# Kernel tuning notes

Measured on AMD Instinct MI355X. Metric: run time of the kernel, lower is better.

Reference implementation:

```python
import jax, jax.numpy as jnp
import numpy as np

TOP_K = 2
EPS = 1e-9


def setup_inputs() -> dict:
    key = jax.random.key(0)
    ks = jax.random.split(key, 5)
    B, S, D, H, E, G = 4, 2048, 1024, 1024, 8, 256
    x = jax.random.normal(ks[0], (B, S, D), dtype=jnp.float32)
    # gate MLP (top_k_gating with hidden_size=gating_size)
    Wg1 = jax.random.normal(ks[1], (D, G), dtype=jnp.float32) * (1.0 / np.sqrt(D))
    Wg2 = jax.random.normal(ks[2], (G, E), dtype=jnp.float32) * (1.0 / np.sqrt(G))
    # experts: uniform(-1/D, 1/D) as in init_experts
    W_in = jax.random.uniform(ks[3], (E, D, H), dtype=jnp.float32, minval=-1.0 / D, maxval=1.0 / D)
    W_out = jax.random.uniform(ks[4], (E, H, D), dtype=jnp.float32, minval=-1.0 / D, maxval=1.0 / D)
    return {"x": x, "Wg1": Wg1, "Wg2": Wg2, "W_in": W_in, "W_out": W_out}


def _gate(xf, Wg1, Wg2):
    # gate MLP -> softmax probs over experts
    h = jnp.tanh(xf @ Wg1)                      # [N, G]
    probs = jax.nn.softmax(h @ Wg2, axis=-1)    # [N, E]
    top_v, top_i = jax.lax.top_k(probs, TOP_K)  # [N, k]
    N, E = probs.shape
    # dense gate matrix: zeros except top-k entries (== compute_gating combine weights)
    gates = jnp.zeros((N, E), probs.dtype).at[jnp.arange(N)[:, None], top_i].set(top_v)
    return gates, probs


def _mi_loss(probs):
    # mutual-information aux loss: minimize -(H(mean_p) - mean H(p))
    p_mean = probs.mean(axis=0)
    h_mean = -jnp.sum(p_mean * jnp.log(p_mean + EPS))
    mean_h = -jnp.mean(jnp.sum(probs * jnp.log(probs + EPS), axis=-1))
    return -h_mean + mean_h


def reference(x, Wg1, Wg2, W_in, W_out):
    B, S, D = x.shape
    xf = x.reshape(-1, D)                        # [N, D]
    gates, probs = _gate(xf, Wg1, Wg2)           # [N, E]
    # per-expert FFN: relu(x @ W_in[e]) @ W_out[e], combined with top-k gates.
    h = jnp.einsum('nd,edh->enh', xf, W_in)      # [E, N, H]
    h = jax.nn.relu(h)
    y = jnp.einsum('enh,ehd->end', h, W_out)     # [E, N, D]
    out = jnp.einsum('ne,end->nd', gates, y)     # gate-weighted combine
    loss = _mi_loss(probs)
    return out.reshape(B, S, D), loss
```

## Files before the change

### kernel.cpp

```cpp
#include <hip/hip_runtime.h>


#define N_TOK 8192
#define DIM   1024
#define HID   1024
#define NEXP  8
#define GDIM  256
#define NPAIR (N_TOK * 2)
#define HB_ROWS (NPAIR + 256)
#define MT2   72
#define GAP_P 5e-4f
#define SPLIT_SCALE 2048.0f

typedef __attribute__((ext_vector_type(4))) float    f32x4;
typedef __attribute__((ext_vector_type(8))) _Float16 f16x8;

static __device__ __forceinline__ void async_ld16(const void* g, void* l) {
  __builtin_amdgcn_global_load_lds(
      (const __attribute__((address_space(1))) unsigned int*)g,
      (__attribute__((address_space(3))) unsigned int*)l, 16, 0, 0);
}

__global__ __launch_bounds__(256) void prep_kernel(const float* __restrict__ x,
                                                   _Float16* __restrict__ xh,
                                                   _Float16* __restrict__ xl,
                                                   const float* __restrict__ Wg1,
                                                   _Float16* __restrict__ WhT,
                                                   _Float16* __restrict__ WlT,
                                                   const float* __restrict__ Win,
                                                   const float* __restrict__ Wout,
                                                   _Float16* __restrict__ WinT,
                                                   _Float16* __restrict__ WoutT) {
  __shared__ float t[64][65];
  int bx = blockIdx.x;
  int tid = threadIdx.x;
  if (bx < 4096) {
    size_t o = ((size_t)bx * 256 + tid) * 8;
    float4 v0 = *(const float4*)(x + o);
    float4 v1 = *(const float4*)(x + o + 4);
    float v[8] = {v0.x, v0.y, v0.z, v0.w, v1.x, v1.y, v1.z, v1.w};
    f16x8 h, l;
#pragma unroll
    for (int k = 0; k < 8; ++k) {
      _Float16 hi = (_Float16)v[k];
      h[k] = hi;
      l[k] = (_Float16)((v[k] - (float)hi) * SPLIT_SCALE);
    }
    *(f16x8*)(xh + o) = h;
    *(f16x8*)(xl + o) = l;
  } else if (bx < 4096 + 64) {
    int b = bx - 4096;
    int k0 = (b & 15) * 64, g0 = (b >> 4) * 64;
    int col4 = tid & 15, ib = tid >> 4;
#pragma unroll
    for (int q = 0; q < 4; ++q) {
      int i = ib * 4 + q;
      *(float4*)&t[i][col4 * 4] = *(const float4*)&Wg1[(size_t)(k0 + i) * GDIM + g0 + col4 * 4];
    }
    __syncthreads();
#pragma unroll
    for (int q = 0; q < 2; ++q) {
      int c = tid * 2 + q;
      int j = c >> 3, i8 = (c & 7) * 8;
      f16x8 h, l;
#pragma unroll
      for (int k = 0; k < 8; ++k) {
        float v = t[i8 + k][j];
        _Float16 hi = (_Float16)v;
        h[k] = hi;
        l[k] = (_Float16)((v - (float)hi) * SPLIT_SCALE);
      }
      *(f16x8*)&WhT[(size_t)(g0 + j) * DIM + k0 + i8] = h;
      *(f16x8*)&WlT[(size_t)(g0 + j) * DIM + k0 + i8] = l;
    }
  } else {
    int b = bx - 4160;
    int z = b >> 8, rem = b & 255;
    const float* src = (z < NEXP ? Win : Wout) + (size_t)(z & 7) * DIM * HID;
    _Float16*    dst = (z < NEXP ? WinT : WoutT) + (size_t)(z & 7) * DIM * HID;
    int i0 = (rem & 15) * 64, j0 = (rem >> 4) * 64;
    int col4 = tid & 15, ib = tid >> 4;
#pragma unroll
    for (int q = 0; q < 4; ++q) {
      int i = ib * 4 + q;
      *(float4*)&t[i][col4 * 4] = *(const float4*)&src[(size_t)(i0 + i) * 1024 + j0 + col4 * 4];
    }
    __syncthreads();
#pragma unroll
    for (int q = 0; q < 2; ++q) {
      int c = tid * 2 + q;
      int j = c >> 3, i8 = (c & 7) * 8;
      f16x8 h;
#pragma unroll
      for (int k = 0; k < 8; ++k) h[k] = (_Float16)t[i8 + k][j];
      *(f16x8*)&dst[(size_t)(j0 + j) * 1024 + i0 + i8] = h;
    }
  }
}

__global__ __launch_bounds__(256) void gemm_hm_kernel(const _Float16* __restrict__ xh,
                                                      const _Float16* __restrict__ xl,
                                                      const _Float16* __restrict__ WhT,
                                                      const _Float16* __restrict__ WlT,
                                                      float* __restrict__ hg) {
  __shared__ __align__(16) _Float16 Ah[32 * 32], Al[32 * 32];
  __shared__ __align__(16) _Float16 Bh[128 * 32], Bl[128 * 32];
  int m0 = blockIdx.x * 32, n0 = blockIdx.y * 128;
  int tid = threadIdx.x, lane = tid & 63, wave = tid >> 6;
  int wr = (wave >> 1) * 16, wc = (wave & 1) * 64;
  int sel = tid >> 7, tt = tid & 127;
  int arow = tt >> 2;
  int aslot = (tt & 3) ^ ((tt >> 4) & 3);
  const _Float16* asrcp = (sel ? xl : xh) + (size_t)(m0 + arow) * DIM + aslot * 8;
  _Float16* adst = (sel ? Al : Ah) + (size_t)tt * 8;
  int brow = tid >> 2;
  int bslot = (tid & 3) ^ ((tid >> 4) & 3);
  size_t boff = (size_t)(n0 + brow) * DIM + bslot * 8;
  const size_t bo2 = (size_t)64 * DIM;
  int rdoff = ((lane >> 4) ^ ((lane >> 2) & 3)) << 3;
  f32x4 acc[4] = {}, accl[4] = {};
  for (int k0 = 0; k0 < DIM; k0 += 32) {
    __syncthreads();
    async_ld16(asrcp + k0, adst);
    async_ld16(WhT + boff + k0, Bh + (size_t)tid * 8);
    async_ld16(WhT + boff + bo2 + k0, Bh + (size_t)(256 + tid) * 8);
    async_ld16(WlT + boff + k0, Bl + (size_t)tid * 8);
    async_ld16(WlT + boff + bo2 + k0, Bl + (size_t)(256 + tid) * 8);
    __syncthreads();
    f16x8 a  = *(const f16x8*)&Ah[(wr + (lane & 15)) * 32 + rdoff];
    f16x8 al = *(const f16x8*)&Al[(wr + (lane & 15)) * 32 + rdoff];
#pragma unroll
    for (int n = 0; n < 4; ++n) {
      f16x8 b  = *(const f16x8*)&Bh[(wc + n * 16 + (lane & 15)) * 32 + rdoff];
      f16x8 bl = *(const f16x8*)&Bl[(wc + n * 16 + (lane & 15)) * 32 + rdoff];
      acc[n]  = __builtin_amdgcn_mfma_f32_16x16x32_f16(a, b, acc[n], 0, 0, 0);
      accl[n] = __builtin_amdgcn_mfma_f32_16x16x32_f16(al, b, accl[n], 0, 0, 0);
      accl[n] = __builtin_amdgcn_mfma_f32_16x16x32_f16(a, bl, accl[n], 0, 0, 0);
    }
  }
#pragma unroll
  for (int n = 0; n < 4; ++n) {
#pragma unroll
    for (int i = 0; i < 4; ++i) {
      int row = wr + ((lane >> 4) << 2) + i;
      int col = wc + n * 16 + (lane & 15);
      float v = acc[n][i] + accl[n][i] * (1.0f / SPLIT_SCALE);
      hg[(size_t)(m0 + row) * GDIM + n0 + col] = tanhf(v);
    }
  }
}

__global__ void gate_kernel(const float* __restrict__ hg, const float* __restrict__ Wg2,
                            int* __restrict__ top_i, float* __restrict__ top_v,
                            float* __restrict__ lossacc, int* __restrict__ counts,
                            int* __restrict__ nflag, int* __restrict__ flaglist) {
  __shared__ float psum[8];
  __shared__ float entsum;
  __shared__ int cnts[8];
  int tid = threadIdx.x;
  if (tid < 8) { psum[tid] = 0.f; cnts[tid] = 0; }
  if (tid == 0) entsum = 0.f;
  __syncthreads();
  int token = blockIdx.x * 8 + (tid >> 5);
  int lane = tid & 31;
  const float* hrow = hg + (size_t)token * GDIM;
  float lg[8] = {0, 0, 0, 0, 0, 0, 0, 0};
#pragma unroll
  for (int j = 0; j < 8; ++j) {
    int g = lane + (j << 5);
    float hv = hrow[g];
#pragma unroll
    for (int e = 0; e < 8; ++e) lg[e] = fmaf(hv, Wg2[g * 8 + e], lg[e]);
  }
#pragma unroll
  for (int e = 0; e < 8; ++e) {
    lg[e] += __shfl_xor(lg[e], 16);
    lg[e] += __shfl_xor(lg[e], 8);
    lg[e] += __shfl_xor(lg[e], 4);
    lg[e] += __shfl_xor(lg[e], 2);
    lg[e] += __shfl_xor(lg[e], 1);
  }
  if (lane == 0) {
    float mx = lg[0];
#pragma unroll
    for (int e = 1; e < 8; ++e) mx = fmaxf(mx, lg[e]);
    float p[8], s = 0.f;
#pragma unroll
    for (int e = 0; e < 8; ++e) { p[e] = expf(lg[e] - mx); s += p[e]; }
    float inv = 1.f / s, ent = 0.f;
    int i0 = 0, i1 = 0;
    float v0 = -1.f, v1 = -1.f, v2 = -1.f;
#pragma unroll
    for (int e = 0; e < 8; ++e) {
      p[e] *= inv;
      ent += p[e] * logf(p[e] + 1e-9f);
      if (p[e] > v0)      { v2 = v1; v1 = v0; i1 = i0; v0 = p[e]; i0 = e; }
      else if (p[e] > v1) { v2 = v1; v1 = p[e]; i1 = e; }
      else if (p[e] > v2) { v2 = p[e]; }
    }
    top_i[token * 2 + 0] = i0; top_i[token * 2 + 1] = i1;
    top_v[token * 2 + 0] = v0; top_v[token * 2 + 1] = v1;
    if (v1 - v2 < GAP_P) {
      int ix = atomicAdd(nflag, 1);
      if (ix < 8192) flaglist[ix] = token;
    }
#pragma unroll
    for (int e = 0; e < 8; ++e) atomicAdd(&psum[e], p[e]);
    atomicAdd(&entsum, ent);
    atomicAdd(&cnts[i0], 1);
    atomicAdd(&cnts[i1], 1);
  }
  __syncthreads();
  if (tid < 8) { atomicAdd(&lossacc[tid], psum[tid]); atomicAdd(&counts[tid], cnts[tid]); }
  if (tid == 8) atomicAdd(&lossacc[8], entsum);
}

__global__ __launch_bounds__(256) void regate_kernel(const float* __restrict__ x,
                                                     const float* __restrict__ Wg1,
                                                     const float* __restrict__ Wg2,
                                                     const int* __restrict__ nflag,
                                                     const int* __restrict__ flaglist,
                                                     int* __restrict__ top_i,
                                                     float* __restrict__ top_v,
                                                     int* __restrict__ counts) {
  __shared__ float xs[DIM];
  __shared__ float wsum[4][8];
  int tid = threadIdx.x;
  int nf = *nflag; if (nf > 8192) nf = 8192;
  for (int it = blockIdx.x; it < nf; it += gridDim.x) {
    int token = flaglist[it];
    const float* xr = x + (size_t)token * DIM;
    *(float4*)&xs[tid * 4] = *(const float4*)&xr[tid * 4];
    __syncthreads();
    float s0 = 0.f, s1 = 0.f, s2 = 0.f, s3 = 0.f;
    float s4 = 0.f, s5 = 0.f, s6 = 0.f, s7 = 0.f;
    for (int k = 0; k < DIM; k += 8) {
      s0 = fmaf(xs[k + 0], Wg1[(size_t)(k + 0) * GDIM + tid], s0);
      s1 = fmaf(xs[k + 1], Wg1[(size_t)(k + 1) * GDIM + tid], s1);
      s2 = fmaf(xs[k + 2], Wg1[(size_t)(k + 2) * GDIM + tid], s2);
      s3 = fmaf(xs[k + 3], Wg1[(size_t)(k + 3) * GDIM + tid], s3);
      s4 = fmaf(xs[k + 4], Wg1[(size_t)(k + 4) * GDIM + tid], s4);
      s5 = fmaf(xs[k + 5], Wg1[(size_t)(k + 5) * GDIM + tid], s5);
      s6 = fmaf(xs[k + 6], Wg1[(size_t)(k + 6) * GDIM + tid], s6);
      s7 = fmaf(xs[k + 7], Wg1[(size_t)(k + 7) * GDIM + tid], s7);
    }
    float hgv = tanhf(((s0 + s1) + (s2 + s3)) + ((s4 + s5) + (s6 + s7)));
    float lg[8];
#pragma unroll
    for (int e = 0; e < 8; ++e) lg[e] = hgv * Wg2[tid * 8 + e];
#pragma unroll
    for (int e = 0; e < 8; ++e) {
      lg[e] += __shfl_xor(lg[e], 32);
      lg[e] += __shfl_xor(lg[e], 16);
      lg[e] += __shfl_xor(lg[e], 8);
      lg[e] += __shfl_xor(lg[e], 4);
      lg[e] += __shfl_xor(lg[e], 2);
      lg[e] += __shfl_xor(lg[e], 1);
    }
    int wv = tid >> 6;
    if ((tid & 63) == 0) {
#pragma unroll
      for (int e = 0; e < 8; ++e) wsum[wv][e] = lg[e];
    }
    __syncthreads();
    if (tid == 0) {
      float l[8];
#pragma unroll
      for (int e = 0; e < 8; ++e)
        l[e] = (wsum[0][e] + wsum[1][e]) + (wsum[2][e] + wsum[3][e]);
      float mx = l[0];
#pragma unroll
      for (int e = 1; e < 8; ++e) mx = fmaxf(mx, l[e]);
      float p[8], s = 0.f;
#pragma unroll
      for (int e = 0; e < 8; ++e) { p[e] = expf(l[e] - mx); s += p[e]; }
      float inv = 1.f / s;
      int i0 = 0, i1 = 0;
      float v0 = -1.f, v1 = -1.f;
#pragma unroll
      for (int e = 0; e < 8; ++e) {
        p[e] *= inv;
        if (p[e] > v0)      { v1 = v0; i1 = i0; v0 = p[e]; i0 = e; }
        else if (p[e] > v1) { v1 = p[e]; i1 = e; }
      }
      int oi0 = top_i[token * 2 + 0], oi1 = top_i[token * 2 + 1];
      if (oi0 != i0 || oi1 != i1) {
        atomicSub(&counts[oi0], 1); atomicSub(&counts[oi1], 1);
        atomicAdd(&counts[i0], 1);  atomicAdd(&counts[i1], 1);
      }
      top_i[token * 2 + 0] = i0; top_i[token * 2 + 1] = i1;
      top_v[token * 2 + 0] = v0; top_v[token * 2 + 1] = v1;
    }
    __syncthreads();
  }
}

__global__ __launch_bounds__(256) void fill_kernel(const int* __restrict__ top_i,
                                                   const float* __restrict__ top_v,
                                                   const int* __restrict__ counts,
                                                   int* __restrict__ cursors,
                                                   int* __restrict__ ptok,
                                                   float* __restrict__ pgate,
                                                   int* __restrict__ rowof) {
  __shared__ int lcnt[8];
  __shared__ int lbase[8];
  __shared__ int soff[8];
  int tid = threadIdx.x;
  int n = blockIdx.x * 256 + tid;
  if (tid == 0) {
    int a = 0;
#pragma unroll
    for (int e = 0; e < 8; ++e) { soff[e] = a; a += counts[e]; }
  }
  if (tid < 8) lcnt[tid] = 0;
  __syncthreads();
  int e0 = top_i[n * 2 + 0], e1 = top_i[n * 2 + 1];
  int p0 = atomicAdd(&lcnt[e0], 1);
  int p1 = atomicAdd(&lcnt[e1], 1);
  __syncthreads();
  if (tid < 8) lbase[tid] = atomicAdd(&cursors[tid], lcnt[tid]);
  __syncthreads();
  int r0 = soff[e0] + lbase[e0] + p0;
  int r1 = soff[e1] + lbase[e1] + p1;
  ptok[r0] = n;  pgate[r0] = top_v[n * 2 + 0];  rowof[n * 2 + 0] = r0;
  ptok[r1] = n;  pgate[r1] = top_v[n * 2 + 1];  rowof[n * 2 + 1] = r1;
}


#define GEMM_PIPE(STAGE_EXPR)                                                        \
  STAGE_EXPR(0, 0);                                                                  \
  STAGE_EXPR(32, 1);                                                                 \
  asm volatile("s_waitcnt vmcnt(3)" ::: "memory");                                   \
  __builtin_amdgcn_s_barrier();                                                      \
  int cbuf = 0;                                                                      \
  for (int t = 0; t < 32; ++t) {                                                     \
    f16x8 a[4], b[4];                                                                \
    _Pragma("unroll")                                                                \
    for (int m = 0; m < 4; ++m)                                                      \
      a[m] = *(const f16x8*)&Als[cbuf][(wr + m * 16 + (lane & 15)) * 32 + rdoff];    \
    _Pragma("unroll")                                                                \
    for (int n = 0; n < 4; ++n)                                                      \
      b[n] = *(const f16x8*)&Bls[cbuf][(wc + n * 16 + (lane & 15)) * 32 + rdoff];    \
    asm volatile("s_waitcnt lgkmcnt(0)" ::: "memory");                               \
    __builtin_amdgcn_sched_barrier(0);                                               \
    __builtin_amdgcn_s_barrier();                                                    \
    bool st = (t + 2 < 32);                                                          \
    if (st) { STAGE_EXPR((t + 2) * 32, cbuf); }                                      \
    __builtin_amdgcn_s_setprio(1);                                                   \
    _Pragma("unroll")                                                                \
    for (int m = 0; m < 4; ++m)                                                      \
      _Pragma("unroll")                                                              \
      for (int n = 0; n < 4; ++n)                                                    \
        acc[m][n] = __builtin_amdgcn_mfma_f32_16x16x32_f16(a[m], b[n], acc[m][n], 0, 0, 0); \
    __builtin_amdgcn_s_setprio(0);                                                   \
    if (st) asm volatile("s_waitcnt vmcnt(3)" ::: "memory");                         \
    else    asm volatile("s_waitcnt vmcnt(0)" ::: "memory");                         \
    __builtin_amdgcn_sched_barrier(0);                                               \
    __builtin_amdgcn_s_barrier();                                                    \
    cbuf ^= 1;                                                                       \
  }

__global__ __launch_bounds__(512) void gemm1_kernel(const _Float16* __restrict__ xh,
                                                    const _Float16* __restrict__ WinT,
                                                    _Float16* __restrict__ hb,
                                                    const int* __restrict__ counts,
                                                    const int* __restrict__ ptok) {
  __shared__ __align__(16) _Float16 Als[2][256 * 32];
  __shared__ __align__(16) _Float16 Bls[2][128 * 32];
  int bx = blockIdx.x;
  int loc = (bx & 7) * 9 + (bx >> 3);
  int base = 0, cnt = 0, e;
  for (e = 0; e < NEXP; ++e) {
    cnt = counts[e];
    int mts = (cnt + 255) >> 8;
    if (loc < mts) break;
    loc -= mts; base += cnt;
  }
  if (e == NEXP) return;
  int row0 = base + (loc << 8);
  int rmax = cnt - (loc << 8);
  int n0 = blockIdx.y << 7;
  int tid = threadIdx.x, wave = tid >> 6, lane = tid & 63;
  int wr = (wave >> 1) << 6, wc = (wave & 1) << 6;

  const _Float16* WB = WinT + (size_t)e * DIM * HID;
  int scol = (((lane & 3) ^ (lane >> 4)) << 3);
  size_t asrc[2];
#pragma unroll
  for (int j = 0; j < 2; ++j) {
    int r = wave * 32 + j * 16 + (lane >> 2);
    int tok = ptok[(r < rmax) ? (row0 + r) : base];
    asrc[j] = (size_t)tok * DIM + scol;
  }
  int brow = tid >> 2;
  size_t bsrc = (size_t)(n0 + brow) * DIM + (((tid & 3) ^ ((tid >> 4) & 3)) << 3);
  int aldst = wave * 1024;
  int bldst = wave * 512;
  int rdoff = ((lane >> 4) ^ ((lane >> 2) & 3)) << 3;
  f32x4 acc[4][4] = {};

#define STAGE1(K0, CB)                                          \
  do {                                                          \
    async_ld16(xh + asrc[0] + (K0), &Als[(CB)][aldst]);         \
    async_ld16(xh + asrc[1] + (K0), &Als[(CB)][aldst + 512]);   \
    async_ld16(WB + bsrc + (K0), &Bls[(CB)][bldst]);            \
  } while (0)

  GEMM_PIPE(STAGE1)
#undef STAGE1

#pragma unroll
  for (int m = 0; m < 4; ++m) {
#pragma unroll
    for (int i = 0; i < 4; ++i) {
      int r = wr + m * 16 + ((lane >> 4) << 2) + i;
      if (r < rmax) {
        _Float16* hrow = hb + (size_t)(row0 + r) * HID;
#pragma unroll
        for (int n = 0; n < 4; ++n)
          hrow[n0 + wc + n * 16 + (lane & 15)] = (_Float16)fmaxf(acc[m][n][i], 0.f);
      }
    }
  }
}

__global__ __launch_bounds__(512) void gemm2_kernel(const _Float16* __restrict__ hb,
                                                    const _Float16* __restrict__ WoutT,
                                                    _Float16* __restrict__ yb,
                                                    const int* __restrict__ counts,
                                                    const float* __restrict__ pgate) {
  __shared__ __align__(16) _Float16 Als[2][256 * 32];
  __shared__ __align__(16) _Float16 Bls[2][128 * 32];
  int bx = blockIdx.x;
  int loc = (bx & 7) * 9 + (bx >> 3);
  int base = 0, cnt = 0, e;
  for (e = 0; e < NEXP; ++e) {
    cnt = counts[e];
    int mts = (cnt + 255) >> 8;
    if (loc < mts) break;
    loc -= mts; base += cnt;
  }
  if (e == NEXP) return;
  int row0 = base + (loc << 8);
  int rmax = cnt - (loc << 8);
  int n0 = blockIdx.y << 7;
  int tid = threadIdx.x, wave = tid >> 6, lane = tid & 63;
  int wr = (wave >> 1) << 6, wc = (wave & 1) << 6;

  const _Float16* WB = WoutT + (size_t)e * DIM * HID;
  int scol = (((lane & 3) ^ (lane >> 4)) << 3);
  size_t asrc[2];
#pragma unroll
  for (int j = 0; j < 2; ++j) {
    int r = wave * 32 + j * 16 + (lane >> 2);
    asrc[j] = (size_t)(row0 + r) * HID + scol;
  }
  int brow = tid >> 2;
  size_t bsrc = (size_t)(n0 + brow) * DIM + (((tid & 3) ^ ((tid >> 4) & 3)) << 3);
  int aldst = wave * 1024;
  int bldst = wave * 512;
  int rdoff = ((lane >> 4) ^ ((lane >> 2) & 3)) << 3;
  f32x4 acc[4][4] = {};

#define STAGE2(K0, CB)                                          \
  do {                                                          \
    async_ld16(hb + asrc[0] + (K0), &Als[(CB)][aldst]);         \
    async_ld16(hb + asrc[1] + (K0), &Als[(CB)][aldst + 512]);   \
    async_ld16(WB + bsrc + (K0), &Bls[(CB)][bldst]);            \
  } while (0)

  GEMM_PIPE(STAGE2)
#undef STAGE2

#pragma unroll
  for (int m = 0; m < 4; ++m) {
#pragma unroll
    for (int i = 0; i < 4; ++i) {
      int r = wr + m * 16 + ((lane >> 4) << 2) + i;
      if (r < rmax) {
        int gr = row0 + r;
        float gv = pgate[gr];
        _Float16* yrow = yb + (size_t)gr * DIM;
#pragma unroll
        for (int n = 0; n < 4; ++n)
          yrow[n0 + wc + n * 16 + (lane & 15)] = (_Float16)(gv * acc[m][n][i]);
      }
    }
  }
}

__global__ __launch_bounds__(256) void combine_kernel(const _Float16* __restrict__ yb,
                                                      const int* __restrict__ rowof,
                                                      float* __restrict__ out,
                                                      const float* __restrict__ lossacc,
                                                      float* __restrict__ lossdst) {
  int tid = threadIdx.x;
  int token = blockIdx.x * 2 + (tid >> 7);
  int d0 = (tid & 127) * 8;
  int r0 = rowof[token * 2 + 0];
  int r1 = rowof[token * 2 + 1];
  f16x8 a = *(const f16x8*)&yb[(size_t)r0 * DIM + d0];
  f16x8 b = *(const f16x8*)&yb[(size_t)r1 * DIM + d0];
  float* orow = out + (size_t)token * DIM + d0;
  float4 o0, o1;
  o0.x = (float)a[0] + (float)b[0]; o0.y = (float)a[1] + (float)b[1];
  o0.z = (float)a[2] + (float)b[2]; o0.w = (float)a[3] + (float)b[3];
  o1.x = (float)a[4] + (float)b[4]; o1.y = (float)a[5] + (float)b[5];
  o1.z = (float)a[6] + (float)b[6]; o1.w = (float)a[7] + (float)b[7];
  *(float4*)orow = o0;
  *(float4*)(orow + 4) = o1;
  if (blockIdx.x == 0 && tid == 0) {
    float t1 = 0.f;
#pragma unroll
    for (int e = 0; e < 8; ++e) {
      float pm = lossacc[e] * (1.f / (float)N_TOK);
      t1 += pm * logf(pm + 1e-9f);
    }
    lossdst[0] = t1 - lossacc[8] * (1.f / (float)N_TOK);
  }
}

extern "C" void kernel_launch(void* const* d_in, const int* in_sizes, int n_in,
                              void* d_out, int out_size, void* d_ws, size_t ws_size,
                              hipStream_t stream) {
  const float* x    = (const float*)d_in[0];
  const float* Wg1  = (const float*)d_in[1];
  const float* Wg2  = (const float*)d_in[2];
  const float* Win  = (const float*)d_in[3];
  const float* Wout = (const float*)d_in[4];
  float* out = (float*)d_out;

  char* ws = (char*)d_ws;
  size_t off = 0;
  auto alloc = [&](size_t bytes) -> void* {
    void* p = ws + off;
    off = (off + bytes + 255) & ~(size_t)255;
    return p;
  };
  int*   counts  = (int*)alloc(32);
  int*   cursors = (int*)alloc(32);
  float* lossacc = (float*)alloc(64);
  int*   nflag   = (int*)alloc(32);
  int*   flaglist= (int*)alloc(8192 * 4);
  int*   top_i   = (int*)alloc((size_t)NPAIR * 4);
  float* top_v   = (float*)alloc((size_t)NPAIR * 4);
  int*   ptok    = (int*)alloc((size_t)NPAIR * 4);
  float* pgate   = (float*)alloc((size_t)NPAIR * 4);
  int*   rowof   = (int*)alloc((size_t)NPAIR * 4);
  float* hg      = (float*)alloc((size_t)N_TOK * GDIM * 4);
  char*  scratch1 = (char*)alloc((size_t)HB_ROWS * HID * 2);
  _Float16* xl     = (_Float16*)scratch1;
  _Float16* Wg1hT  = (_Float16*)(scratch1 + (size_t)N_TOK * DIM * 2);
  _Float16* Wg1lsT = Wg1hT + (size_t)GDIM * DIM;
  _Float16* hb     = (_Float16*)scratch1;
  _Float16* xh    = (_Float16*)alloc((size_t)N_TOK * DIM * 2);
  _Float16* WinT  = (_Float16*)alloc((size_t)NEXP * DIM * HID * 2);
  _Float16* WoutT = (_Float16*)alloc((size_t)NEXP * DIM * HID * 2);
  _Float16* yb = xh;
  (void)ws_size; (void)in_sizes; (void)n_in;

  hipMemsetAsync(d_ws, 0, 2048, stream);

  prep_kernel<<<4096 + 64 + 4096, 256, 0, stream>>>(x, xh, xl, Wg1, Wg1hT, Wg1lsT,
                                                    Win, Wout, WinT, WoutT);
  gemm_hm_kernel<<<dim3(N_TOK / 32, GDIM / 128), 256, 0, stream>>>(xh, xl, Wg1hT, Wg1lsT, hg);
  gate_kernel<<<N_TOK / 8, 256, 0, stream>>>(hg, Wg2, top_i, top_v, lossacc, counts,
                                             nflag, flaglist);
  regate_kernel<<<256, 256, 0, stream>>>(x, Wg1, Wg2, nflag, flaglist, top_i, top_v, counts);
  fill_kernel<<<N_TOK / 256, 256, 0, stream>>>(top_i, top_v, counts, cursors,
                                               ptok, pgate, rowof);
  gemm1_kernel<<<dim3(MT2, HID / 128), 512, 0, stream>>>(xh, WinT, hb, counts, ptok);
  gemm2_kernel<<<dim3(MT2, DIM / 128), 512, 0, stream>>>(hb, WoutT, yb, counts, pgate);
  combine_kernel<<<N_TOK / 2, 256, 0, stream>>>(yb, rowof, out, lossacc,
                                                out + (size_t)N_TOK * DIM);
}
```

Before: 261.5 us.

## Halve GEMM workgroup to 4 waves with 128x64 per-wave tiles

Both expert GEMM kernels now use 256 threads (4 waves) instead of 512 for the same 256x128 block tile. Each wave computes a 128x64 sub-tile with 8x4 MFMA accumulators and issues six async loads per stage, and the vmcnt waits are updated to match. The aim is more register-level reuse of A/B fragments per LDS read and fewer waves synchronising at barriers. The cost is doubled accumulator register pressure, which with launch_bounds(256,2) may limit occupancy or cause spills.

```diff
diff --git a/kernel.cpp b/kernel.cpp
--- a/kernel.cpp
+++ b/kernel.cpp
@@ -330,13 +330,13 @@
 #define GEMM_PIPE(STAGE_EXPR)                                                        \
   STAGE_EXPR(0, 0);                                                                  \
   STAGE_EXPR(32, 1);                                                                 \
-  asm volatile("s_waitcnt vmcnt(3)" ::: "memory");                                   \
+  asm volatile("s_waitcnt vmcnt(6)" ::: "memory");                                   \
   __builtin_amdgcn_s_barrier();                                                      \
   int cbuf = 0;                                                                      \
   for (int t = 0; t < 32; ++t) {                                                     \
-    f16x8 a[4], b[4];                                                                \
+    f16x8 a[8], b[4];                                                                \
     _Pragma("unroll")                                                                \
-    for (int m = 0; m < 4; ++m)                                                      \
+    for (int m = 0; m < 8; ++m)                                                      \
       a[m] = *(const f16x8*)&Als[cbuf][(wr + m * 16 + (lane & 15)) * 32 + rdoff];    \
     _Pragma("unroll")                                                                \
     for (int n = 0; n < 4; ++n)                                                      \
@@ -348,23 +348,23 @@
     if (st) { STAGE_EXPR((t + 2) * 32, cbuf); }                                      \
     __builtin_amdgcn_s_setprio(1);                                                   \
     _Pragma("unroll")                                                                \
-    for (int m = 0; m < 4; ++m)                                                      \
+    for (int m = 0; m < 8; ++m)                                                      \
       _Pragma("unroll")                                                              \
       for (int n = 0; n < 4; ++n)                                                    \
         acc[m][n] = __builtin_amdgcn_mfma_f32_16x16x32_f16(a[m], b[n], acc[m][n], 0, 0, 0); \
     __builtin_amdgcn_s_setprio(0);                                                   \
-    if (st) asm volatile("s_waitcnt vmcnt(3)" ::: "memory");                         \
+    if (st) asm volatile("s_waitcnt vmcnt(6)" ::: "memory");                         \
     else    asm volatile("s_waitcnt vmcnt(0)" ::: "memory");                         \
     __builtin_amdgcn_sched_barrier(0);                                               \
     __builtin_amdgcn_s_barrier();                                                    \
     cbuf ^= 1;                                                                       \
   }
 
-__global__ __launch_bounds__(512) void gemm1_kernel(const _Float16* __restrict__ xh,
-                                                    const _Float16* __restrict__ WinT,
-                                                    _Float16* __restrict__ hb,
-                                                    const int* __restrict__ counts,
-                                                    const int* __restrict__ ptok) {
+__global__ __launch_bounds__(256, 2) void gemm1_kernel(const _Float16* __restrict__ xh,
+                                                       const _Float16* __restrict__ WinT,
+                                                       _Float16* __restrict__ hb,
+                                                       const int* __restrict__ counts,
+                                                       const int* __restrict__ ptok) {
   __shared__ __align__(16) _Float16 Als[2][256 * 32];
   __shared__ __align__(16) _Float16 Bls[2][128 * 32];
   int bx = blockIdx.x;
@@ -381,36 +381,42 @@
   int rmax = cnt - (loc << 8);
   int n0 = blockIdx.y << 7;
   int tid = threadIdx.x, wave = tid >> 6, lane = tid & 63;
-  int wr = (wave >> 1) << 6, wc = (wave & 1) << 6;
+  int wr = (wave >> 1) << 7;
+  int wc = (wave & 1) << 6;
 
   const _Float16* WB = WinT + (size_t)e * DIM * HID;
   int scol = (((lane & 3) ^ (lane >> 4)) << 3);
-  size_t asrc[2];
-#pragma unroll
-  for (int j = 0; j < 2; ++j) {
-    int r = wave * 32 + j * 16 + (lane >> 2);
+  size_t asrc[4];
+#pragma unroll
+  for (int j = 0; j < 4; ++j) {
+    int r = wave * 64 + j * 16 + (lane >> 2);
     int tok = ptok[(r < rmax) ? (row0 + r) : base];
     asrc[j] = (size_t)tok * DIM + scol;
   }
-  int brow = tid >> 2;
-  size_t bsrc = (size_t)(n0 + brow) * DIM + (((tid & 3) ^ ((tid >> 4) & 3)) << 3);
-  int aldst = wave * 1024;
-  int bldst = wave * 512;
+  size_t bsrc[2];
+#pragma unroll
+  for (int j = 0; j < 2; ++j) {
+    int r = j * 64 + (tid >> 2);
+    bsrc[j] = (size_t)(n0 + r) * DIM + (((tid & 3) ^ ((tid >> 4) & 3)) << 3);
+  }
   int rdoff = ((lane >> 4) ^ ((lane >> 2) & 3)) << 3;
-  f32x4 acc[4][4] = {};
-
-#define STAGE1(K0, CB)                                          \
-  do {                                                          \
-    async_ld16(xh + asrc[0] + (K0), &Als[(CB)][aldst]);         \
-    async_ld16(xh + asrc[1] + (K0), &Als[(CB)][aldst + 512]);   \
-    async_ld16(WB + bsrc + (K0), &Bls[(CB)][bldst]);            \
+  f32x4 acc[8][4] = {};
+
+#define STAGE1(K0, CB)                                                 \
+  do {                                                                 \
+    async_ld16(xh + asrc[0] + (K0), &Als[(CB)][wave * 2048]);          \
+    async_ld16(xh + asrc[1] + (K0), &Als[(CB)][wave * 2048 + 512]);    \
+    async_ld16(xh + asrc[2] + (K0), &Als[(CB)][wave * 2048 + 1024]);   \
+    async_ld16(xh + asrc[3] + (K0), &Als[(CB)][wave * 2048 + 1536]);   \
+    async_ld16(WB + bsrc[0] + (K0), &Bls[(CB)][wave * 512]);           \
+    async_ld16(WB + bsrc[1] + (K0), &Bls[(CB)][2048 + wave * 512]);    \
   } while (0)
 
   GEMM_PIPE(STAGE1)
 #undef STAGE1
 
 #pragma unroll
-  for (int m = 0; m < 4; ++m) {
+  for (int m = 0; m < 8; ++m) {
 #pragma unroll
     for (int i = 0; i < 4; ++i) {
       int r = wr + m * 16 + ((lane >> 4) << 2) + i;
@@ -424,11 +430,11 @@
   }
 }
 
-__global__ __launch_bounds__(512) void gemm2_kernel(const _Float16* __restrict__ hb,
-                                                    const _Float16* __restrict__ WoutT,
-                                                    _Float16* __restrict__ yb,
-                                                    const int* __restrict__ counts,
-                                                    const float* __restrict__ pgate) {
+__global__ __launch_bounds__(256, 2) void gemm2_kernel(const _Float16* __restrict__ hb,
+                                                       const _Float16* __restrict__ WoutT,
+                                                       _Float16* __restrict__ yb,
+                                                       const int* __restrict__ counts,
+                                                       const float* __restrict__ pgate) {
   __shared__ __align__(16) _Float16 Als[2][256 * 32];
   __shared__ __align__(16) _Float16 Bls[2][128 * 32];
   int bx = blockIdx.x;
@@ -445,35 +451,40 @@
   int rmax = cnt - (loc << 8);
   int n0 = blockIdx.y << 7;
   int tid = threadIdx.x, wave = tid >> 6, lane = tid & 63;
-  int wr = (wave >> 1) << 6, wc = (wave & 1) << 6;
+  int wr = (wave >> 1) << 7, wc = (wave & 1) << 6;
 
   const _Float16* WB = WoutT + (size_t)e * DIM * HID;
   int scol = (((lane & 3) ^ (lane >> 4)) << 3);
-  size_t asrc[2];
+  size_t asrc[4];
+#pragma unroll
+  for (int j = 0; j < 4; ++j) {
+    int r = wave * 64 + j * 16 + (lane >> 2);
+    asrc[j] = (size_t)(row0 + r) * HID + scol;
+  }
+  size_t bsrc[2];
 #pragma unroll
   for (int j = 0; j < 2; ++j) {
-    int r = wave * 32 + j * 16 + (lane >> 2);
-    asrc[j] = (size_t)(row0 + r) * HID + scol;
-  }
-  int brow = tid >> 2;
-  size_t bsrc = (size_t)(n0 + brow) * DIM + (((tid & 3) ^ ((tid >> 4) & 3)) << 3);
-  int aldst = wave * 1024;
-  int bldst = wave * 512;
+    int r = j * 64 + (tid >> 2);
+    bsrc[j] = (size_t)(n0 + r) * DIM + (((tid & 3) ^ ((tid >> 4) & 3)) << 3);
+  }
   int rdoff = ((lane >> 4) ^ ((lane >> 2) & 3)) << 3;
-  f32x4 acc[4][4] = {};
-
-#define STAGE2(K0, CB)                                          \
-  do {                                                          \
-    async_ld16(hb + asrc[0] + (K0), &Als[(CB)][aldst]);         \
-    async_ld16(hb + asrc[1] + (K0), &Als[(CB)][aldst + 512]);   \
-    async_ld16(WB + bsrc + (K0), &Bls[(CB)][bldst]);            \
+  f32x4 acc[8][4] = {};
+
+#define STAGE2(K0, CB)                                                 \
+  do {                                                                 \
+    async_ld16(hb + asrc[0] + (K0), &Als[(CB)][wave * 2048]);          \
+    async_ld16(hb + asrc[1] + (K0), &Als[(CB)][wave * 2048 + 512]);    \
+    async_ld16(hb + asrc[2] + (K0), &Als[(CB)][wave * 2048 + 1024]);   \
+    async_ld16(hb + asrc[3] + (K0), &Als[(CB)][wave * 2048 + 1536]);   \
+    async_ld16(WB + bsrc[0] + (K0), &Bls[(CB)][wave * 512]);           \
+    async_ld16(WB + bsrc[1] + (K0), &Bls[(CB)][2048 + wave * 512]);    \
   } while (0)
 
   GEMM_PIPE(STAGE2)
 #undef STAGE2
 
 #pragma unroll
-  for (int m = 0; m < 4; ++m) {
+  for (int m = 0; m < 8; ++m) {
 #pragma unroll
     for (int i = 0; i < 4; ++i) {
       int r = wr + m * 16 + ((lane >> 4) << 2) + i;
@@ -569,8 +580,8 @@
   regate_kernel<<<256, 256, 0, stream>>>(x, Wg1, Wg2, nflag, flaglist, top_i, top_v, counts);
   fill_kernel<<<N_TOK / 256, 256, 0, stream>>>(top_i, top_v, counts, cursors,
                                                ptok, pgate, rowof);
-  gemm1_kernel<<<dim3(MT2, HID / 128), 512, 0, stream>>>(xh, WinT, hb, counts, ptok);
-  gemm2_kernel<<<dim3(MT2, DIM / 128), 512, 0, stream>>>(hb, WoutT, yb, counts, pgate);
+  gemm1_kernel<<<dim3(MT2, HID / 128), 256, 0, stream>>>(xh, WinT, hb, counts, ptok);
+  gemm2_kernel<<<dim3(MT2, DIM / 128), 256, 0, stream>>>(hb, WoutT, yb, counts, pgate);
   combine_kernel<<<N_TOK / 2, 256, 0, stream>>>(yb, rowof, out, lossacc,
                                                 out + (size_t)N_TOK * DIM);
 }
```

Result: no change. 265.8 us (+1.6%).

## Fuse gate GEMM with gate softmax, drop x low-part split, fold memset into prep

Applied to the files above, without the earlier changes.

Merges the gating GEMM and gate/top-k kernel so each block computes a 32x256 tile of tanh(x@Wg1), keeps it in shared memory and does the Wg2 projection, softmax and top-k in place. The hg round-trip through global memory and one launch go away. The x low-part (xl) split is dropped, so the gate GEMM uses x in fp16 with only Wg1 split into high and low parts, removing one MFMA per step and the xl writes. To absorb the lost precision, the near-tie threshold for regating is raised from 5e-4 to 2e-3, so more tokens go to the exact fp32 regate path. The hipMemset is replaced by an extra prep block that zeroes the header.

```diff
diff --git a/kernel.cpp b/kernel.cpp
--- a/kernel.cpp
+++ b/kernel.cpp
@@ -9,8 +9,9 @@
 #define NPAIR (N_TOK * 2)
 #define HB_ROWS (NPAIR + 256)
 #define MT2   72
-#define GAP_P 5e-4f
+#define GAP_P 2e-3f
 #define SPLIT_SCALE 2048.0f
+#define NPREP (4096 + 64 + 4096)
 
 typedef __attribute__((ext_vector_type(4))) float    f32x4;
 typedef __attribute__((ext_vector_type(8))) _Float16 f16x8;
@@ -23,14 +24,14 @@
 
 __global__ __launch_bounds__(256) void prep_kernel(const float* __restrict__ x,
                                                    _Float16* __restrict__ xh,
-                                                   _Float16* __restrict__ xl,
                                                    const float* __restrict__ Wg1,
                                                    _Float16* __restrict__ WhT,
                                                    _Float16* __restrict__ WlT,
                                                    const float* __restrict__ Win,
                                                    const float* __restrict__ Wout,
                                                    _Float16* __restrict__ WinT,
-                                                   _Float16* __restrict__ WoutT) {
+                                                   _Float16* __restrict__ WoutT,
+                                                   int* __restrict__ hdr) {
   __shared__ float t[64][65];
   int bx = blockIdx.x;
   int tid = threadIdx.x;
@@ -39,15 +40,10 @@
     float4 v0 = *(const float4*)(x + o);
     float4 v1 = *(const float4*)(x + o + 4);
     float v[8] = {v0.x, v0.y, v0.z, v0.w, v1.x, v1.y, v1.z, v1.w};
-    f16x8 h, l;
-#pragma unroll
-    for (int k = 0; k < 8; ++k) {
-      _Float16 hi = (_Float16)v[k];
-      h[k] = hi;
-      l[k] = (_Float16)((v[k] - (float)hi) * SPLIT_SCALE);
-    }
+    f16x8 h;
+#pragma unroll
+    for (int k = 0; k < 8; ++k) h[k] = (_Float16)v[k];
     *(f16x8*)(xh + o) = h;
-    *(f16x8*)(xl + o) = l;
   } else if (bx < 4096 + 64) {
     int b = bx - 4096;
     int k0 = (b & 15) * 64, g0 = (b >> 4) * 64;
@@ -73,7 +69,7 @@
       *(f16x8*)&WhT[(size_t)(g0 + j) * DIM + k0 + i8] = h;
       *(f16x8*)&WlT[(size_t)(g0 + j) * DIM + k0 + i8] = l;
     }
-  } else {
+  } else if (bx < NPREP) {
     int b = bx - 4160;
     int z = b >> 8, rem = b & 255;
     const float* src = (z < NEXP ? Win : Wout) + (size_t)(z & 7) * DIM * HID;
@@ -95,92 +91,91 @@
       for (int k = 0; k < 8; ++k) h[k] = (_Float16)t[i8 + k][j];
       *(f16x8*)&dst[(size_t)(j0 + j) * 1024 + i0 + i8] = h;
     }
-  }
-}
-
-__global__ __launch_bounds__(256) void gemm_hm_kernel(const _Float16* __restrict__ xh,
-                                                      const _Float16* __restrict__ xl,
-                                                      const _Float16* __restrict__ WhT,
-                                                      const _Float16* __restrict__ WlT,
-                                                      float* __restrict__ hg) {
-  __shared__ __align__(16) _Float16 Ah[32 * 32], Al[32 * 32];
-  __shared__ __align__(16) _Float16 Bh[128 * 32], Bl[128 * 32];
-  int m0 = blockIdx.x * 32, n0 = blockIdx.y * 128;
+  } else {
+    hdr[tid * 2 + 0] = 0;
+    hdr[tid * 2 + 1] = 0;
+  }
+}
+
+__global__ __launch_bounds__(256) void gemm_gate_kernel(const _Float16* __restrict__ xh,
+                                                        const _Float16* __restrict__ WhT,
+                                                        const _Float16* __restrict__ WlT,
+                                                        const float* __restrict__ Wg2,
+                                                        int* __restrict__ top_i,
+                                                        float* __restrict__ top_v,
+                                                        float* __restrict__ lossacc,
+                                                        int* __restrict__ counts,
+                                                        int* __restrict__ nflag,
+                                                        int* __restrict__ flaglist) {
+  __shared__ __align__(16) _Float16 Ah[32 * 32];
+  __shared__ __align__(16) _Float16 Bh[256 * 32];
+  __shared__ __align__(16) _Float16 Bl[256 * 32];
+  __shared__ float hsm[32][260];
+  __shared__ float psum[8];
+  __shared__ float entsum;
+  __shared__ int cnts[8];
+  int m0 = blockIdx.x * 32;
   int tid = threadIdx.x, lane = tid & 63, wave = tid >> 6;
-  int wr = (wave >> 1) * 16, wc = (wave & 1) * 64;
-  int sel = tid >> 7, tt = tid & 127;
-  int arow = tt >> 2;
-  int aslot = (tt & 3) ^ ((tt >> 4) & 3);
-  const _Float16* asrcp = (sel ? xl : xh) + (size_t)(m0 + arow) * DIM + aslot * 8;
-  _Float16* adst = (sel ? Al : Ah) + (size_t)tt * 8;
-  int brow = tid >> 2;
-  int bslot = (tid & 3) ^ ((tid >> 4) & 3);
-  size_t boff = (size_t)(n0 + brow) * DIM + bslot * 8;
-  const size_t bo2 = (size_t)64 * DIM;
+  int wr = (wave >> 1) * 16;
+  int wc = (wave & 1) * 128;
+  if (tid < 8) { psum[tid] = 0.f; cnts[tid] = 0; }
+  if (tid == 0) entsum = 0.f;
+
+  int srcslot = ((lane & 3) ^ ((lane >> 4) & 3)) << 3;
+  size_t asrc = (size_t)(m0 + wave * 16 + (lane >> 2)) * DIM + srcslot;
+  size_t bsrc[4];
+#pragma unroll
+  for (int p = 0; p < 4; ++p)
+    bsrc[p] = (size_t)(wave * 16 + p * 64 + (lane >> 2)) * DIM + srcslot;
   int rdoff = ((lane >> 4) ^ ((lane >> 2) & 3)) << 3;
-  f32x4 acc[4] = {}, accl[4] = {};
+  f32x4 acc[8] = {}, accl[8] = {};
+
   for (int k0 = 0; k0 < DIM; k0 += 32) {
     __syncthreads();
-    async_ld16(asrcp + k0, adst);
-    async_ld16(WhT + boff + k0, Bh + (size_t)tid * 8);
-    async_ld16(WhT + boff + bo2 + k0, Bh + (size_t)(256 + tid) * 8);
-    async_ld16(WlT + boff + k0, Bl + (size_t)tid * 8);
-    async_ld16(WlT + boff + bo2 + k0, Bl + (size_t)(256 + tid) * 8);
-    __syncthreads();
-    f16x8 a  = *(const f16x8*)&Ah[(wr + (lane & 15)) * 32 + rdoff];
-    f16x8 al = *(const f16x8*)&Al[(wr + (lane & 15)) * 32 + rdoff];
-#pragma unroll
-    for (int n = 0; n < 4; ++n) {
-      f16x8 b  = *(const f16x8*)&Bh[(wc + n * 16 + (lane & 15)) * 32 + rdoff];
+    if (wave < 2) async_ld16(xh + asrc + k0, Ah + wave * 512);
+#pragma unroll
+    for (int p = 0; p < 4; ++p) {
+      async_ld16(WhT + bsrc[p] + k0, Bh + wave * 512 + p * 2048);
+      async_ld16(WlT + bsrc[p] + k0, Bl + wave * 512 + p * 2048);
+    }
+    __syncthreads();
+    f16x8 a = *(const f16x8*)&Ah[(wr + (lane & 15)) * 32 + rdoff];
+#pragma unroll
+    for (int n = 0; n < 8; ++n) {
+      f16x8 bh = *(const f16x8*)&Bh[(wc + n * 16 + (lane & 15)) * 32 + rdoff];
       f16x8 bl = *(const f16x8*)&Bl[(wc + n * 16 + (lane & 15)) * 32 + rdoff];
-      acc[n]  = __builtin_amdgcn_mfma_f32_16x16x32_f16(a, b, acc[n], 0, 0, 0);
-      accl[n] = __builtin_amdgcn_mfma_f32_16x16x32_f16(al, b, accl[n], 0, 0, 0);
+      acc[n]  = __builtin_amdgcn_mfma_f32_16x16x32_f16(a, bh, acc[n], 0, 0, 0);
       accl[n] = __builtin_amdgcn_mfma_f32_16x16x32_f16(a, bl, accl[n], 0, 0, 0);
     }
   }
 #pragma unroll
-  for (int n = 0; n < 4; ++n) {
+  for (int n = 0; n < 8; ++n) {
 #pragma unroll
     for (int i = 0; i < 4; ++i) {
       int row = wr + ((lane >> 4) << 2) + i;
       int col = wc + n * 16 + (lane & 15);
-      float v = acc[n][i] + accl[n][i] * (1.0f / SPLIT_SCALE);
-      hg[(size_t)(m0 + row) * GDIM + n0 + col] = tanhf(v);
-    }
-  }
-}
-
-__global__ void gate_kernel(const float* __restrict__ hg, const float* __restrict__ Wg2,
-                            int* __restrict__ top_i, float* __restrict__ top_v,
-                            float* __restrict__ lossacc, int* __restrict__ counts,
-                            int* __restrict__ nflag, int* __restrict__ flaglist) {
-  __shared__ float psum[8];
-  __shared__ float entsum;
-  __shared__ int cnts[8];
-  int tid = threadIdx.x;
-  if (tid < 8) { psum[tid] = 0.f; cnts[tid] = 0; }
-  if (tid == 0) entsum = 0.f;
+      hsm[row][col] = tanhf(acc[n][i] + accl[n][i] * (1.0f / SPLIT_SCALE));
+    }
+  }
   __syncthreads();
-  int token = blockIdx.x * 8 + (tid >> 5);
-  int lane = tid & 31;
-  const float* hrow = hg + (size_t)token * GDIM;
+
+  int tok = tid >> 3, sl = tid & 7;
   float lg[8] = {0, 0, 0, 0, 0, 0, 0, 0};
 #pragma unroll
-  for (int j = 0; j < 8; ++j) {
-    int g = lane + (j << 5);
-    float hv = hrow[g];
+  for (int j = 0; j < 32; ++j) {
+    int g = sl + j * 8;
+    float hv = hsm[tok][g];
 #pragma unroll
     for (int e = 0; e < 8; ++e) lg[e] = fmaf(hv, Wg2[g * 8 + e], lg[e]);
   }
 #pragma unroll
   for (int e = 0; e < 8; ++e) {
-    lg[e] += __shfl_xor(lg[e], 16);
-    lg[e] += __shfl_xor(lg[e], 8);
     lg[e] += __shfl_xor(lg[e], 4);
     lg[e] += __shfl_xor(lg[e], 2);
     lg[e] += __shfl_xor(lg[e], 1);
   }
-  if (lane == 0) {
+  if (sl == 0) {
+    int token = m0 + tok;
     float mx = lg[0];
 #pragma unroll
     for (int e = 1; e < 8; ++e) mx = fmaxf(mx, lg[e]);
@@ -325,7 +320,6 @@
   ptok[r0] = n;  pgate[r0] = top_v[n * 2 + 0];  rowof[n * 2 + 0] = r0;
   ptok[r1] = n;  pgate[r1] = top_v[n * 2 + 1];  rowof[n * 2 + 1] = r1;
 }
-
 
 #define GEMM_PIPE(STAGE_EXPR)                                                        \
   STAGE_EXPR(0, 0);                                                                  \
@@ -547,10 +541,8 @@
   int*   ptok    = (int*)alloc((size_t)NPAIR * 4);
   float* pgate   = (float*)alloc((size_t)NPAIR * 4);
   int*   rowof   = (int*)alloc((size_t)NPAIR * 4);
-  float* hg      = (float*)alloc((size_t)N_TOK * GDIM * 4);
   char*  scratch1 = (char*)alloc((size_t)HB_ROWS * HID * 2);
-  _Float16* xl     = (_Float16*)scratch1;
-  _Float16* Wg1hT  = (_Float16*)(scratch1 + (size_t)N_TOK * DIM * 2);
+  _Float16* Wg1hT  = (_Float16*)scratch1;
   _Float16* Wg1lsT = Wg1hT + (size_t)GDIM * DIM;
   _Float16* hb     = (_Float16*)scratch1;
   _Float16* xh    = (_Float16*)alloc((size_t)N_TOK * DIM * 2);
@@ -559,13 +551,10 @@
   _Float16* yb = xh;
   (void)ws_size; (void)in_sizes; (void)n_in;
 
-  hipMemsetAsync(d_ws, 0, 2048, stream);
-
-  prep_kernel<<<4096 + 64 + 4096, 256, 0, stream>>>(x, xh, xl, Wg1, Wg1hT, Wg1lsT,
-                                                    Win, Wout, WinT, WoutT);
-  gemm_hm_kernel<<<dim3(N_TOK / 32, GDIM / 128), 256, 0, stream>>>(xh, xl, Wg1hT, Wg1lsT, hg);
-  gate_kernel<<<N_TOK / 8, 256, 0, stream>>>(hg, Wg2, top_i, top_v, lossacc, counts,
-                                             nflag, flaglist);
+  prep_kernel<<<NPREP + 1, 256, 0, stream>>>(x, xh, Wg1, Wg1hT, Wg1lsT,
+                                             Win, Wout, WinT, WoutT, (int*)d_ws);
+  gemm_gate_kernel<<<N_TOK / 32, 256, 0, stream>>>(xh, Wg1hT, Wg1lsT, Wg2, top_i, top_v,
+                                                   lossacc, counts, nflag, flaglist);
   regate_kernel<<<256, 256, 0, stream>>>(x, Wg1, Wg2, nflag, flaglist, top_i, top_v, counts);
   fill_kernel<<<N_TOK / 256, 256, 0, stream>>>(top_i, top_v, counts, cursors,
                                                ptok, pgate, rowof);
```

Result: faster. 255.7 us (-2.2%).
